# Performance work log

Measured on AMD Instinct MI355X. Metric: run time of the kernel, lower is better.

Reference implementation:

```python
import jax, jax.numpy as jnp
import numpy as np

N = 50000   # input points
E = 800000  # edges
M = 25000   # sampled points (ratio 0.5)
K = 15      # num_neighbors
H = 128     # hidden_dim
BN_EPS = 1e-5


def setup_inputs() -> dict:
    key = jax.random.key(0)
    ks = jax.random.split(key, 16)
    w = lambda k, s: jax.random.normal(k, s, dtype=jnp.float32) * 0.02
    z = lambda s: jnp.zeros(s, jnp.float32)
    o = lambda s: jnp.ones(s, jnp.float32)
    return {
        'points': jax.random.normal(ks[0], (N, 3), jnp.float32),
        'edge_index': jax.random.randint(ks[1], (2, E), 0, N),
        'sampled_idx': jnp.sort(jax.random.randint(ks[2], (M,), 0, N)),
        'neighbors': jax.random.randint(ks[3], (M, K), 0, M),
        'W1': w(ks[4], (3, H)), 'b1': z(H), 'g1': o(H), 'beta1': z(H),
        'W2': w(ks[5], (H, H)), 'b2': z(H), 'g2': o(H), 'beta2': z(H),
        'Wc': w(ks[6], (H, H)), 'bc': z(H),
        'Wn': w(ks[7], (H, H)), 'bn_b': z(H),
        'Wq': w(ks[8], (H, H // 2)), 'bq': z(H // 2),
        'Wk': w(ks[9], (H, H // 2)), 'bk': z(H // 2),
        'Wcat': w(ks[10], (H + 3, H + 3)), 'bcat': z(H + 3),
        'Wout': w(ks[11], (H + 3, 3)), 'bout': z(3),
    }


def _bn(x, g, b):
    # BatchNorm1d in training mode: batch mean, biased batch var
    m = x.mean(axis=0)
    v = x.var(axis=0)
    return g * (x - m) * jax.lax.rsqrt(v + BN_EPS) + b


def reference(points, edge_index, sampled_idx, neighbors,
              W1, b1, g1, beta1, W2, b2, g2, beta2,
              Wc, bc, Wn, bn_b, Wq, bq, Wk, bk, Wcat, bcat, Wout, bout):
    n = points.shape[0]
    # PointMLP x2: Linear -> BN -> ReLU
    x = jax.nn.relu(_bn(points @ W1 + b1, g1, beta1))
    x = jax.nn.relu(_bn(x @ W2 + b2, g2, beta2))
    # CustomGNN: relu(W_c x + mean_{j in N(i)} W_n x_j)
    src, dst = edge_index[0], edge_index[1]
    msg = (x @ Wn + bn_b)[src]                                   # [E, H]
    agg = jax.ops.segment_sum(msg, dst, num_segments=n)          # [N, H]
    cnt = jax.ops.segment_sum(jnp.ones(src.shape, jnp.float32), dst, num_segments=n)
    agg = agg / jnp.maximum(cnt, 1.0)[:, None]
    x = jax.nn.relu(x @ Wc + bc + agg)
    # sampling (indices precomputed, like fps output)
    sp = points[sampled_idx]                                     # [M, 3]
    sx = x[sampled_idx]                                          # [M, H]
    # AttentionLayer, fully vectorized over sampled points
    q = sx @ Wq + bq                                             # [M, H/2]
    nb_x = sx[neighbors]                                         # [M, K, H]
    k = nb_x @ Wk + bk                                           # [M, K, H/2]
    scale = jnp.sqrt(jnp.float32(q.shape[-1])) + 1e-6
    scores = jnp.einsum('md,mkd->mk', q, k) / scale              # [M, K]
    mask = (neighbors != 0).astype(jnp.float32)                  # quirk preserved
    attn = jax.nn.softmax(scores * mask, axis=1)                 # [M, K]
    rel = sp[neighbors] - sp[:, None, :]                         # [M, K, 3]
    cat = jnp.concatenate([nb_x, rel], axis=-1)                  # [M, K, H+3]
    proc = cat @ Wcat + bcat                                     # [M, K, H+3]
    aggf = jnp.einsum('mk,mkd->md', attn, proc)                  # [M, H+3]
    disp = aggf @ Wout + bout                                    # [M, 3]
    refined = sp + disp
    return refined, sx
```

## Files before the change

### kernel.cpp

```cpp
#include <hip/hip_runtime.h>
#include <climits>

#define NPTS 50000
#define NE   800000
#define MS   25000
#define KN   15
#define HD   128

__device__ __forceinline__ float wave_sum(float v) {
#pragma unroll
    for (int o = 32; o > 0; o >>= 1) v += __shfl_xor(v, o, 64);
    return v;
}

__launch_bounds__(256)
__global__ void prep_kernel(const float* __restrict__ Wq, const float* __restrict__ bq,
                            const float* __restrict__ Wk, const float* __restrict__ bk,
                            const float* __restrict__ Wcat, const float* __restrict__ bcat,
                            const float* __restrict__ Wout, const float* __restrict__ bout,
                            const float* __restrict__ Wc, const float* __restrict__ Wn,
                            float* __restrict__ Wqk, float* __restrict__ biasQK,
                            float* __restrict__ WcWn,
                            float* __restrict__ Wco128, float* __restrict__ w3, float* __restrict__ bco,
                            int* __restrict__ inv, int* __restrict__ cnt, int* __restrict__ cursor) {
    int b = blockIdx.x, tid = threadIdx.x;
    if (b < 64) {
        int i = b * 256 + tid;
        int k = i >> 7, c = i & 127;
        Wqk[i] = (c < 64) ? Wq[k * 64 + c] : Wk[k * 64 + (c - 64)];
    } else if (b < 192) {
        int i = (b - 64) * 256 + tid;
        int k = i >> 7, c = i & 127;
        WcWn[i] = (k < 128) ? Wc[k * 128 + c] : Wn[(k - 128) * 128 + c];
    } else if (b == 192) {
        if (tid < 128) biasQK[tid] = (tid < 64) ? bq[tid] : bk[tid - 64];
    } else if (b < 293) {
        int wid = tid >> 6, lane = tid & 63;
        int out = (b - 193) * 4 + wid;
        if (out < 396) {
            int r = out / 3, j = out - r * 3;
            const float* src = (r < 131) ? &Wcat[r * 131] : bcat;
            float s = 0.f;
            s = fmaf(src[lane], Wout[lane * 3 + j], s);
            s = fmaf(src[lane + 64], Wout[(lane + 64) * 3 + j], s);
            if (lane < 3) s = fmaf(src[lane + 128], Wout[(lane + 128) * 3 + j], s);
            s = wave_sum(s);
            if (lane == 0) {
                if (r < 128) Wco128[r * 3 + j] = s;
                else if (r < 131) w3[(r - 128) * 3 + j] = s;
                else bco[j] = s + bout[j];
            }
        }
    } else {
        int i = (b - 293) * 256 + tid;
        if (i < NPTS) inv[i] = INT_MAX;
        if (i < MS) { cnt[i] = 0; cursor[i] = 0; }
    }
}

__launch_bounds__(256)
__global__ void lin1_kernel(const float* __restrict__ pts, const float* __restrict__ W1,
                            const float* __restrict__ b1, float* __restrict__ y1,
                            float* __restrict__ psum, float* __restrict__ psq,
                            const int* __restrict__ smp, int* __restrict__ inv) {
    if (blockIdx.x >= 1000) {
        int m = (blockIdx.x - 1000) * 256 + threadIdx.x;
        if (m < MS) atomicMin(&inv[smp[m]], m);
        return;
    }
    int c = threadIdx.x & 127;
    int half = threadIdx.x >> 7;
    int part = blockIdx.x * 2 + half;
    float w0 = W1[c], w1 = W1[128 + c], w2 = W1[256 + c], bb = b1[c];
    float s = 0.f, s2 = 0.f;
    int r0 = part * 25, r1 = r0 + 25; if (r1 > NPTS) r1 = NPTS;
    for (int r = r0; r < r1; ++r) {
        float p0 = pts[r * 3], p1 = pts[r * 3 + 1], p2 = pts[r * 3 + 2];
        float y = fmaf(p0, w0, fmaf(p1, w1, fmaf(p2, w2, bb)));
        y1[r * HD + c] = y;
        s += y; s2 = fmaf(y, y, s2);
    }
    psum[part * 128 + c] = s;
    psq[part * 128 + c] = s2;
}

__launch_bounds__(256)
__global__ void bn_fin_par(const float* __restrict__ psum, const float* __restrict__ psq, int nb,
                           const float* __restrict__ g, const float* __restrict__ beta,
                           float* __restrict__ tp) {
    int c = blockIdx.x;
    int t = threadIdx.x;
    float S = 0.f, S2 = 0.f;
    for (int b = t; b < nb; b += 256) {
        S += psum[b * 128 + c];
        S2 += psq[b * 128 + c];
    }
    S = wave_sum(S); S2 = wave_sum(S2);
    __shared__ float sA[4], sB[4];
    int wid = t >> 6, lane = t & 63;
    if (lane == 0) { sA[wid] = S; sB[wid] = S2; }
    __syncthreads();
    if (t == 0) {
        float Sa = sA[0] + sA[1] + sA[2] + sA[3];
        float Sb = sB[0] + sB[1] + sB[2] + sB[3];
        const float invN = 1.f / (float)NPTS;
        float mean = Sa * invN;
        float var = Sb * invN - mean * mean;
        float a = g[c] * rsqrtf(var + 1e-5f);
        tp[c] = a;
        tp[128 + c] = beta[c] - mean * a;
    }
}

template <int R, bool TRANS, bool STATS, bool COUNT>
__launch_bounds__(256)
__global__ void gemm_bn(const float* __restrict__ A, int nrows, int gemmBlocks,
                        const float* __restrict__ W, const float* __restrict__ bias,
                        const float* __restrict__ tp,
                        float* __restrict__ Out,
                        float* __restrict__ psum, float* __restrict__ psq,
                        const int* __restrict__ ei, const int* __restrict__ inv,
                        int* __restrict__ cnt) {
    if (COUNT && (int)blockIdx.x >= gemmBlocks) {
        int e = ((int)blockIdx.x - gemmBlocks) * 256 + threadIdx.x;
        if (e < NE) {
            int mr = inv[ei[NE + e]];
            if (mr < MS) atomicAdd(&cnt[mr], 1);
        }
        return;
    }
    const int ROWS = 8 * R;
    __shared__ float As[8 * R][68];
    __shared__ float Ws[64][128];
    int tid = threadIdx.x;
    int r0 = blockIdx.x * ROWS;
    int tc = tid & 31, tr = tid >> 5;
    int trR = tr * R, c0 = tc << 2;
    float acc[R][4] = {};

    for (int k0 = 0; k0 < 128; k0 += 64) {
        if (k0) __syncthreads();
        for (int i = tid; i < ROWS * 16; i += 256) {
            int r = i >> 4, c4 = (i & 15) << 2;
            int gr = r0 + r;
            float4 v = make_float4(0.f, 0.f, 0.f, 0.f);
            if (gr < nrows) {
                v = *reinterpret_cast<const float4*>(&A[gr * HD + k0 + c4]);
                if (TRANS) {
                    int gc = k0 + c4;
                    v.x = fmaxf(fmaf(tp[gc],     v.x, tp[128 + gc]),     0.f);
                    v.y = fmaxf(fmaf(tp[gc + 1], v.y, tp[128 + gc + 1]), 0.f);
                    v.z = fmaxf(fmaf(tp[gc + 2], v.z, tp[128 + gc + 2]), 0.f);
                    v.w = fmaxf(fmaf(tp[gc + 3], v.w, tp[128 + gc + 3]), 0.f);
                }
            }
            *reinterpret_cast<float4*>(&As[r][c4]) = v;
        }
        for (int i = tid; i < 64 * 32; i += 256) {
            int k = i >> 5, c4 = (i & 31) << 2;
            *reinterpret_cast<float4*>(&Ws[k][c4]) =
                *reinterpret_cast<const float4*>(&W[(k0 + k) * 128 + c4]);
        }
        __syncthreads();
#pragma unroll 2
        for (int k = 0; k < 64; k += 4) {
            float4 a[R];
#pragma unroll
            for (int i = 0; i < R; ++i)
                a[i] = *reinterpret_cast<const float4*>(&As[trR + i][k]);
#pragma unroll
            for (int kk = 0; kk < 4; ++kk) {
                const float4 wv = *reinterpret_cast<const float4*>(&Ws[k + kk][c0]);
#pragma unroll
                for (int i = 0; i < R; ++i) {
                    float av = kk == 0 ? a[i].x : kk == 1 ? a[i].y : kk == 2 ? a[i].z : a[i].w;
                    acc[i][0] = fmaf(av, wv.x, acc[i][0]);
                    acc[i][1] = fmaf(av, wv.y, acc[i][1]);
                    acc[i][2] = fmaf(av, wv.z, acc[i][2]);
                    acc[i][3] = fmaf(av, wv.w, acc[i][3]);
                }
            }
        }
    }

    const float4 bv = *reinterpret_cast<const float4*>(&bias[c0]);
    float cs[4] = {}, cq[4] = {};
#pragma unroll
    for (int i = 0; i < R; ++i) {
        int gr = r0 + trR + i;
        float o0 = acc[i][0] + bv.x, o1 = acc[i][1] + bv.y;
        float o2 = acc[i][2] + bv.z, o3 = acc[i][3] + bv.w;
        if (gr < nrows) {
            *reinterpret_cast<float4*>(&Out[gr * HD + c0]) = make_float4(o0, o1, o2, o3);
            if (STATS) {
                cs[0] += o0; cs[1] += o1; cs[2] += o2; cs[3] += o3;
                cq[0] = fmaf(o0, o0, cq[0]); cq[1] = fmaf(o1, o1, cq[1]);
                cq[2] = fmaf(o2, o2, cq[2]); cq[3] = fmaf(o3, o3, cq[3]);
            }
        }
    }
    if (STATS) {
        float* red = &As[0][0];
        __syncthreads();
        *reinterpret_cast<float4*>(&red[tr * 128 + c0]) = make_float4(cs[0], cs[1], cs[2], cs[3]);
        __syncthreads();
        if (tid < 128) {
            float s = 0.f;
#pragma unroll
            for (int t = 0; t < 8; ++t) s += red[t * 128 + tid];
            psum[blockIdx.x * 128 + tid] = s;
        }
        __syncthreads();
        *reinterpret_cast<float4*>(&red[tr * 128 + c0]) = make_float4(cq[0], cq[1], cq[2], cq[3]);
        __syncthreads();
        if (tid < 128) {
            float s = 0.f;
#pragma unroll
            for (int t = 0; t < 8; ++t) s += red[t * 128 + tid];
            psq[blockIdx.x * 128 + tid] = s;
        }
    }
}

__launch_bounds__(1024)
__global__ void scan_kernel(const int* __restrict__ cnt, int* __restrict__ offs) {
    const int C = 25;
    __shared__ int buf[1024];
    int tid = threadIdx.x;
    int loc[C];
    int run = 0;
    int base = tid * C;
#pragma unroll
    for (int i = 0; i < C; ++i) {
        int idx = base + i;
        int v = (idx < MS) ? cnt[idx] : 0;
        loc[i] = run; run += v;
    }
    buf[tid] = run;
    __syncthreads();
    for (int off = 1; off < 1024; off <<= 1) {
        int t = (tid >= off) ? buf[tid - off] : 0;
        __syncthreads();
        buf[tid] += t;
        __syncthreads();
    }
    int excl = buf[tid] - run;
#pragma unroll
    for (int i = 0; i < C; ++i) {
        int idx = base + i;
        if (idx < MS) offs[idx] = excl + loc[i];
    }
    if (tid == 1023) offs[MS] = buf[tid];
}

__launch_bounds__(256)
__global__ void scatter_kernel(const int* __restrict__ ei, const int* __restrict__ inv,
                               const int* __restrict__ offs, int* __restrict__ cursor,
                               int* __restrict__ elist) {
    int e = blockIdx.x * 256 + threadIdx.x;
    if (e < NE) {
        int mr = inv[ei[NE + e]];
        if (mr < MS) {
            int pos = atomicAdd(&cursor[mr], 1);
            elist[offs[mr] + pos] = ei[e];
        }
    }
}

__launch_bounds__(256)
__global__ void agg_kernel(const int* __restrict__ smp, const int* __restrict__ inv,
                           const int* __restrict__ offs, const int* __restrict__ elist,
                           const float* __restrict__ y2, const float* __restrict__ tp2,
                           float* __restrict__ aggX, float* __restrict__ hasE) {
    int tid = threadIdx.x, wid = tid >> 6, lane = tid & 63;
    int m = blockIdx.x * 4 + wid;
    if (m >= MS) return;
    int d = smp[m];
    if (inv[d] != m) return;
    int half = lane >> 5, c0 = (lane & 31) << 2;
    const float4 ta = *reinterpret_cast<const float4*>(&tp2[c0]);
    const float4 tb = *reinterpret_cast<const float4*>(&tp2[128 + c0]);
    int e0 = offs[m], e1 = offs[m + 1];
    float4 s0 = {0,0,0,0}, s1 = {0,0,0,0}, s2 = {0,0,0,0}, s3 = {0,0,0,0};
    int e = e0;
    for (; e + 7 < e1; e += 8) {
        float4 v[4];
#pragma unroll
        for (int u = 0; u < 4; ++u)
            v[u] = *reinterpret_cast<const float4*>(&y2[elist[e + 2 * u + half] * HD + c0]);
        s0.x += fmaxf(fmaf(ta.x, v[0].x, tb.x), 0.f); s0.y += fmaxf(fmaf(ta.y, v[0].y, tb.y), 0.f);
        s0.z += fmaxf(fmaf(ta.z, v[0].z, tb.z), 0.f); s0.w += fmaxf(fmaf(ta.w, v[0].w, tb.w), 0.f);
        s1.x += fmaxf(fmaf(ta.x, v[1].x, tb.x), 0.f); s1.y += fmaxf(fmaf(ta.y, v[1].y, tb.y), 0.f);
        s1.z += fmaxf(fmaf(ta.z, v[1].z, tb.z), 0.f); s1.w += fmaxf(fmaf(ta.w, v[1].w, tb.w), 0.f);
        s2.x += fmaxf(fmaf(ta.x, v[2].x, tb.x), 0.f); s2.y += fmaxf(fmaf(ta.y, v[2].y, tb.y), 0.f);
        s2.z += fmaxf(fmaf(ta.z, v[2].z, tb.z), 0.f); s2.w += fmaxf(fmaf(ta.w, v[2].w, tb.w), 0.f);
        s3.x += fmaxf(fmaf(ta.x, v[3].x, tb.x), 0.f); s3.y += fmaxf(fmaf(ta.y, v[3].y, tb.y), 0.f);
        s3.z += fmaxf(fmaf(ta.z, v[3].z, tb.z), 0.f); s3.w += fmaxf(fmaf(ta.w, v[3].w, tb.w), 0.f);
    }
    for (; e + 1 < e1; e += 2) {
        const float4 v = *reinterpret_cast<const float4*>(&y2[elist[e + half] * HD + c0]);
        s0.x += fmaxf(fmaf(ta.x, v.x, tb.x), 0.f); s0.y += fmaxf(fmaf(ta.y, v.y, tb.y), 0.f);
        s0.z += fmaxf(fmaf(ta.z, v.z, tb.z), 0.f); s0.w += fmaxf(fmaf(ta.w, v.w, tb.w), 0.f);
    }
    if (e < e1 && half == 0) {
        const float4 v = *reinterpret_cast<const float4*>(&y2[elist[e] * HD + c0]);
        s1.x += fmaxf(fmaf(ta.x, v.x, tb.x), 0.f); s1.y += fmaxf(fmaf(ta.y, v.y, tb.y), 0.f);
        s1.z += fmaxf(fmaf(ta.z, v.z, tb.z), 0.f); s1.w += fmaxf(fmaf(ta.w, v.w, tb.w), 0.f);
    }
    float tx = (s0.x + s1.x) + (s2.x + s3.x);
    float ty = (s0.y + s1.y) + (s2.y + s3.y);
    float tz = (s0.z + s1.z) + (s2.z + s3.z);
    float tw = (s0.w + s1.w) + (s2.w + s3.w);
    tx += __shfl_xor(tx, 32, 64); ty += __shfl_xor(ty, 32, 64);
    tz += __shfl_xor(tz, 32, 64); tw += __shfl_xor(tw, 32, 64);
    float rs = 1.f / fmaxf((float)(e1 - e0), 1.f);
    if (half == 0)
        *reinterpret_cast<float4*>(&aggX[m * HD + c0]) = make_float4(tx * rs, ty * rs, tz * rs, tw * rs);
    if (lane == 0) hasE[m] = (e1 > e0) ? 1.f : 0.f;
}

__launch_bounds__(256)
__global__ void gemm_sx_fused(const float* __restrict__ y2, const float* __restrict__ aggX,
                              const float* __restrict__ hasE,
                              const int* __restrict__ smp, const int* __restrict__ inv,
                              const float* __restrict__ WcWn,
                              const float* __restrict__ bc, const float* __restrict__ bn_b,
                              const float* __restrict__ tp2,
                              const float* __restrict__ Wqk, const float* __restrict__ biasQK,
                              const float* __restrict__ Wco128, const float* __restrict__ pts,
                              float* __restrict__ sx, float* __restrict__ qkb,
                              float* __restrict__ p3, float* __restrict__ sp) {
    const int R = 3;
    __shared__ float As[24][68];
    __shared__ float Ws[64][128];
    __shared__ float sxs[24][132];
    int tid = threadIdx.x;
    int r0 = blockIdx.x * 24;
    int tc = tid & 31, tr = tid >> 5;
    int trR = tr * R, c0 = tc << 2;
    float acc[R][4] = {};

    for (int kk = 0; kk < 4; ++kk) {
        if (kk) __syncthreads();
        for (int i = tid; i < 24 * 16; i += 256) {
            int r = i >> 4, c4 = (i & 15) << 2;
            int gr = r0 + r;
            float4 v = make_float4(0.f, 0.f, 0.f, 0.f);
            if (gr < MS) {
                int d = smp[gr];
                if (kk < 2) {
                    int gc = (kk << 6) + c4;
                    v = *reinterpret_cast<const float4*>(&y2[d * HD + gc]);
                    v.x = fmaxf(fmaf(tp2[gc],     v.x, tp2[128 + gc]),     0.f);
                    v.y = fmaxf(fmaf(tp2[gc + 1], v.y, tp2[128 + gc + 1]), 0.f);
                    v.z = fmaxf(fmaf(tp2[gc + 2], v.z, tp2[128 + gc + 2]), 0.f);
                    v.w = fmaxf(fmaf(tp2[gc + 3], v.w, tp2[128 + gc + 3]), 0.f);
                } else {
                    v = *reinterpret_cast<const float4*>(&aggX[inv[d] * HD + ((kk - 2) << 6) + c4]);
                }
            }
            *reinterpret_cast<float4*>(&As[r][c4]) = v;
        }
        for (int i = tid; i < 64 * 32; i += 256) {
            int k = i >> 5, c4 = (i & 31) << 2;
            *reinterpret_cast<float4*>(&Ws[k][c4]) =
                *reinterpret_cast<const float4*>(&WcWn[((kk << 6) + k) * 128 + c4]);
        }
        __syncthreads();
#pragma unroll 2
        for (int k = 0; k < 64; k += 4) {
            float4 a[R];
#pragma unroll
            for (int i = 0; i < R; ++i)
                a[i] = *reinterpret_cast<const float4*>(&As[trR + i][k]);
#pragma unroll
            for (int kq = 0; kq < 4; ++kq) {
                const float4 wv = *reinterpret_cast<const float4*>(&Ws[k + kq][c0]);
#pragma unroll
                for (int i = 0; i < R; ++i) {
                    float av = kq == 0 ? a[i].x : kq == 1 ? a[i].y : kq == 2 ? a[i].z : a[i].w;
                    acc[i][0] = fmaf(av, wv.x, acc[i][0]);
                    acc[i][1] = fmaf(av, wv.y, acc[i][1]);
                    acc[i][2] = fmaf(av, wv.z, acc[i][2]);
                    acc[i][3] = fmaf(av, wv.w, acc[i][3]);
                }
            }
        }
    }

    {
        const float4 bcv = *reinterpret_cast<const float4*>(&bc[c0]);
        const float4 bnv = *reinterpret_cast<const float4*>(&bn_b[c0]);
#pragma unroll
        for (int i = 0; i < R; ++i) {
            int gr = r0 + trR + i;
            float4 ov = make_float4(0.f, 0.f, 0.f, 0.f);
            if (gr < MS) {
                float f = hasE[inv[smp[gr]]];
                ov.x = fmaxf(acc[i][0] + bcv.x + f * bnv.x, 0.f);
                ov.y = fmaxf(acc[i][1] + bcv.y + f * bnv.y, 0.f);
                ov.z = fmaxf(acc[i][2] + bcv.z + f * bnv.z, 0.f);
                ov.w = fmaxf(acc[i][3] + bcv.w + f * bnv.w, 0.f);
                *reinterpret_cast<float4*>(&sx[gr * HD + c0]) = ov;
            }
            *reinterpret_cast<float4*>(&sxs[trR + i][c0]) = ov;
        }
    }
    __syncthreads();

    float qacc[R][4] = {};
    for (int kk = 0; kk < 2; ++kk) {
        if (kk) __syncthreads();
        for (int i = tid; i < 64 * 32; i += 256) {
            int k = i >> 5, c4 = (i & 31) << 2;
            *reinterpret_cast<float4*>(&Ws[k][c4]) =
                *reinterpret_cast<const float4*>(&Wqk[((kk << 6) + k) * 128 + c4]);
        }
        __syncthreads();
        int kb = kk << 6;
#pragma unroll 2
        for (int k = 0; k < 64; k += 4) {
            float4 a[R];
#pragma unroll
            for (int i = 0; i < R; ++i)
                a[i] = *reinterpret_cast<const float4*>(&sxs[trR + i][kb + k]);
#pragma unroll
            for (int kq = 0; kq < 4; ++kq) {
                const float4 wv = *reinterpret_cast<const float4*>(&Ws[k + kq][c0]);
#pragma unroll
                for (int i = 0; i < R; ++i) {
                    float av = kq == 0 ? a[i].x : kq == 1 ? a[i].y : kq == 2 ? a[i].z : a[i].w;
                    qacc[i][0] = fmaf(av, wv.x, qacc[i][0]);
                    qacc[i][1] = fmaf(av, wv.y, qacc[i][1]);
                    qacc[i][2] = fmaf(av, wv.z, qacc[i][2]);
                    qacc[i][3] = fmaf(av, wv.w, qacc[i][3]);
                }
            }
        }
    }
    {
        const float4 bqv = *reinterpret_cast<const float4*>(&biasQK[c0]);
#pragma unroll
        for (int i = 0; i < R; ++i) {
            int gr = r0 + trR + i;
            if (gr < MS) {
                *reinterpret_cast<float4*>(&qkb[gr * HD + c0]) = make_float4(
                    qacc[i][0] + bqv.x, qacc[i][1] + bqv.y,
                    qacc[i][2] + bqv.z, qacc[i][3] + bqv.w);
            }
        }
    }

    {
        int wid = tid >> 6, lane = tid & 63;
        int cc = lane << 1;
        float wa0 = Wco128[cc * 3],     wa1 = Wco128[cc * 3 + 1],     wa2 = Wco128[cc * 3 + 2];
        float wb0 = Wco128[(cc+1) * 3], wb1 = Wco128[(cc+1) * 3 + 1], wb2 = Wco128[(cc+1) * 3 + 2];
#pragma unroll
        for (int rr = wid * 6; rr < wid * 6 + 6; ++rr) {
            int m = r0 + rr;
            if (m >= MS) break;
            float vx = sxs[rr][cc], vy = sxs[rr][cc + 1];
            float q0 = fmaf(vx, wa0, vy * wb0);
            float q1 = fmaf(vx, wa1, vy * wb1);
            float q2 = fmaf(vx, wa2, vy * wb2);
            q0 = wave_sum(q0); q1 = wave_sum(q1); q2 = wave_sum(q2);
            if (lane == 0) { p3[m * 3] = q0; p3[m * 3 + 1] = q1; p3[m * 3 + 2] = q2; }
            if (lane < 3) sp[m * 3 + lane] = pts[smp[m] * 3 + lane];
        }
    }
}

__launch_bounds__(256)
__global__ void attn_kernel(const float* __restrict__ qk, const int* __restrict__ nbr,
                            const float* __restrict__ p3, const float* __restrict__ sp,
                            const float* __restrict__ w3, const float* __restrict__ bco,
                            float* __restrict__ refined) {
    int wid = threadIdx.x >> 6, lane = threadIdx.x & 63;
    int m = blockIdx.x * 4 + wid;
    if (m >= MS) return;
    float ql = qk[m * HD + lane];
    int nbv[KN];
    float s[KN];
#pragma unroll
    for (int j = 0; j < KN; ++j) nbv[j] = nbr[m * KN + j];
#pragma unroll
    for (int j = 0; j < KN; ++j) {
        float t = ql * qk[nbv[j] * HD + 64 + lane];
        t = wave_sum(t);
        s[j] = (nbv[j] != 0) ? t * (1.f / 8.000001f) : 0.f;
    }
    float mx = s[0];
#pragma unroll
    for (int j = 1; j < KN; ++j) mx = fmaxf(mx, s[j]);
    float den = 0.f;
#pragma unroll
    for (int j = 0; j < KN; ++j) { s[j] = __expf(s[j] - mx); den += s[j]; }
    float invd = 1.f / den;
    float sp0 = sp[m * 3], sp1 = sp[m * 3 + 1], sp2 = sp[m * 3 + 2];
    float a0 = 0.f, a1 = 0.f, a2 = 0.f;
#pragma unroll
    for (int j = 0; j < KN; ++j) {
        int nb = nbv[j];
        float wgt = s[j] * invd;
        float r0 = sp[nb * 3] - sp0, r1 = sp[nb * 3 + 1] - sp1, r2 = sp[nb * 3 + 2] - sp2;
        float g0 = p3[nb * 3]     + r0 * w3[0] + r1 * w3[3] + r2 * w3[6];
        float g1 = p3[nb * 3 + 1] + r0 * w3[1] + r1 * w3[4] + r2 * w3[7];
        float g2 = p3[nb * 3 + 2] + r0 * w3[2] + r1 * w3[5] + r2 * w3[8];
        a0 = fmaf(wgt, g0, a0); a1 = fmaf(wgt, g1, a1); a2 = fmaf(wgt, g2, a2);
    }
    if (lane == 0) {
        refined[m * 3]     = sp0 + a0 + bco[0];
        refined[m * 3 + 1] = sp1 + a1 + bco[1];
        refined[m * 3 + 2] = sp2 + a2 + bco[2];
    }
}

extern "C" void kernel_launch(void* const* d_in, const int* in_sizes, int n_in,
                              void* d_out, int out_size, void* d_ws, size_t ws_size,
                              hipStream_t stream) {
    const float* pts   = (const float*)d_in[0];
    const int*   ei    = (const int*)d_in[1];
    const int*   smp   = (const int*)d_in[2];
    const int*   nbr   = (const int*)d_in[3];
    const float* W1    = (const float*)d_in[4];
    const float* b1    = (const float*)d_in[5];
    const float* g1    = (const float*)d_in[6];
    const float* beta1 = (const float*)d_in[7];
    const float* W2    = (const float*)d_in[8];
    const float* b2    = (const float*)d_in[9];
    const float* g2    = (const float*)d_in[10];
    const float* beta2 = (const float*)d_in[11];
    const float* Wc    = (const float*)d_in[12];
    const float* bc    = (const float*)d_in[13];
    const float* Wn    = (const float*)d_in[14];
    const float* bn_b  = (const float*)d_in[15];
    const float* Wq    = (const float*)d_in[16];
    const float* bq    = (const float*)d_in[17];
    const float* Wk    = (const float*)d_in[18];
    const float* bk    = (const float*)d_in[19];
    const float* Wcat  = (const float*)d_in[20];
    const float* bcat  = (const float*)d_in[21];
    const float* Wout  = (const float*)d_in[22];
    const float* bout  = (const float*)d_in[23];
    (void)in_sizes; (void)n_in; (void)out_size; (void)ws_size;

    float* w = (float*)d_ws;
    size_t o = 0;
    float* y1     = w + o; o += 6400000;
    float* y2     = w + o; o += 6400000;
    float* aggX   = w + o; o += 3200000;
    float* qkb    = w + o; o += 3200000;
    float* psum   = w + o; o += 262144;
    float* psq    = w + o; o += 262144;
    float* tp1    = w + o; o += 256;
    float* tp2    = w + o; o += 256;
    float* Wqk    = w + o; o += 16384;
    float* biasQK = w + o; o += 128;
    float* WcWn   = w + o; o += 32768;
    float* Wco128 = w + o; o += 384;
    float* w3     = w + o; o += 16;
    float* bco    = w + o; o += 16;
    float* p3     = w + o; o += 75008;
    float* sp     = w + o; o += 75008;
    float* hasE   = w + o; o += 25008;
    int* ip    = (int*)(w + o);
    int* inv   = ip;            ip += NPTS;
    int* cnt   = ip;            ip += MS;
    int* cursor= ip;            ip += MS;
    int* offs  = ip;            ip += MS + 4;
    int* elist = ip;

    float* refined = (float*)d_out;
    float* sx      = (float*)d_out + 75000;

    prep_kernel<<<489, 256, 0, stream>>>(Wq, bq, Wk, bk, Wcat, bcat, Wout, bout, Wc, Wn,
                                         Wqk, biasQK, WcWn, Wco128, w3, bco,
                                         inv, cnt, cursor);
    lin1_kernel<<<1098, 256, 0, stream>>>(pts, W1, b1, y1, psum, psq, smp, inv);
    bn_fin_par<<<128, 256, 0, stream>>>(psum, psq, 2000, g1, beta1, tp1);
    gemm_bn<6, true, true, true><<<1042 + 3125, 256, 0, stream>>>(
        y1, NPTS, 1042, W2, b2, tp1, y2, psum, psq, ei, inv, cnt);
    bn_fin_par<<<128, 256, 0, stream>>>(psum, psq, 1042, g2, beta2, tp2);
    scan_kernel<<<1, 1024, 0, stream>>>(cnt, offs);
    scatter_kernel<<<3125, 256, 0, stream>>>(ei, inv, offs, cursor, elist);
    agg_kernel<<<6250, 256, 0, stream>>>(smp, inv, offs, elist, y2, tp2, aggX, hasE);
    gemm_sx_fused<<<1042, 256, 0, stream>>>(y2, aggX, hasE, smp, inv, WcWn, bc, bn_b, tp2,
                                            Wqk, biasQK, Wco128, pts, sx, qkb, p3, sp);
    attn_kernel<<<6250, 256, 0, stream>>>(qkb, nbr, p3, sp, w3, bco, refined);
}
```

Measured before the change: 321.6 us.

## Recompute first linear layer inside second GEMM and enlarge GEMM row tiles

The first point linear layer no longer writes its 50000x128 output; it only produces BN statistics, and the second GEMM recomputes it from the 3-D points on the fly before applying BN and ReLU. This removes a large global write and read of y1 in exchange for a little extra arithmetic per tile load. The y2 GEMM tile grows from 48 to 64 rows and the sx fused GEMM from 24 to 32 rows, reusing the sxs shared buffer as the A tile to save shared memory. The larger tiles raise register pressure and reduce block count.

```diff
diff --git a/kernel.cpp b/kernel.cpp
--- a/kernel.cpp
+++ b/kernel.cpp
@@ -59,10 +59,10 @@
 }
 
 __launch_bounds__(256)
-__global__ void lin1_kernel(const float* __restrict__ pts, const float* __restrict__ W1,
-                            const float* __restrict__ b1, float* __restrict__ y1,
-                            float* __restrict__ psum, float* __restrict__ psq,
-                            const int* __restrict__ smp, int* __restrict__ inv) {
+__global__ void lin1_stats(const float* __restrict__ pts, const float* __restrict__ W1,
+                           const float* __restrict__ b1,
+                           float* __restrict__ psum, float* __restrict__ psq,
+                           const int* __restrict__ smp, int* __restrict__ inv) {
     if (blockIdx.x >= 1000) {
         int m = (blockIdx.x - 1000) * 256 + threadIdx.x;
         if (m < MS) atomicMin(&inv[smp[m]], m);
@@ -77,7 +77,6 @@
     for (int r = r0; r < r1; ++r) {
         float p0 = pts[r * 3], p1 = pts[r * 3 + 1], p2 = pts[r * 3 + 2];
         float y = fmaf(p0, w0, fmaf(p1, w1, fmaf(p2, w2, bb)));
-        y1[r * HD + c] = y;
         s += y; s2 = fmaf(y, y, s2);
     }
     psum[part * 128 + c] = s;
@@ -112,16 +111,16 @@
     }
 }
 
-template <int R, bool TRANS, bool STATS, bool COUNT>
-__launch_bounds__(256)
-__global__ void gemm_bn(const float* __restrict__ A, int nrows, int gemmBlocks,
-                        const float* __restrict__ W, const float* __restrict__ bias,
-                        const float* __restrict__ tp,
-                        float* __restrict__ Out,
+__launch_bounds__(256)
+__global__ void gemm_y2(const float* __restrict__ pts, const float* __restrict__ W1,
+                        const float* __restrict__ b1, const float* __restrict__ tp1,
+                        const float* __restrict__ W2, const float* __restrict__ b2,
+                        int gemmBlocks,
+                        float* __restrict__ y2,
                         float* __restrict__ psum, float* __restrict__ psq,
                         const int* __restrict__ ei, const int* __restrict__ inv,
                         int* __restrict__ cnt) {
-    if (COUNT && (int)blockIdx.x >= gemmBlocks) {
+    if ((int)blockIdx.x >= gemmBlocks) {
         int e = ((int)blockIdx.x - gemmBlocks) * 256 + threadIdx.x;
         if (e < NE) {
             int mr = inv[ei[NE + e]];
@@ -129,50 +128,57 @@
         }
         return;
     }
-    const int ROWS = 8 * R;
-    __shared__ float As[8 * R][68];
+    __shared__ float As[64][68];
     __shared__ float Ws[64][128];
     int tid = threadIdx.x;
-    int r0 = blockIdx.x * ROWS;
+    int r0 = blockIdx.x * 64;
     int tc = tid & 31, tr = tid >> 5;
-    int trR = tr * R, c0 = tc << 2;
-    float acc[R][4] = {};
+    int trR = tr * 8, c0 = tc << 2;
+    float acc[8][4] = {};
 
     for (int k0 = 0; k0 < 128; k0 += 64) {
         if (k0) __syncthreads();
-        for (int i = tid; i < ROWS * 16; i += 256) {
+        for (int i = tid; i < 64 * 16; i += 256) {
             int r = i >> 4, c4 = (i & 15) << 2;
             int gr = r0 + r;
             float4 v = make_float4(0.f, 0.f, 0.f, 0.f);
-            if (gr < nrows) {
-                v = *reinterpret_cast<const float4*>(&A[gr * HD + k0 + c4]);
-                if (TRANS) {
-                    int gc = k0 + c4;
-                    v.x = fmaxf(fmaf(tp[gc],     v.x, tp[128 + gc]),     0.f);
-                    v.y = fmaxf(fmaf(tp[gc + 1], v.y, tp[128 + gc + 1]), 0.f);
-                    v.z = fmaxf(fmaf(tp[gc + 2], v.z, tp[128 + gc + 2]), 0.f);
-                    v.w = fmaxf(fmaf(tp[gc + 3], v.w, tp[128 + gc + 3]), 0.f);
-                }
+            if (gr < NPTS) {
+                int gc = k0 + c4;
+                float p0 = pts[gr * 3], p1 = pts[gr * 3 + 1], p2 = pts[gr * 3 + 2];
+                const float4 wa = *reinterpret_cast<const float4*>(&W1[gc]);
+                const float4 wb = *reinterpret_cast<const float4*>(&W1[128 + gc]);
+                const float4 wc = *reinterpret_cast<const float4*>(&W1[256 + gc]);
+                const float4 bb = *reinterpret_cast<const float4*>(&b1[gc]);
+                const float4 ta = *reinterpret_cast<const float4*>(&tp1[gc]);
+                const float4 tb = *reinterpret_cast<const float4*>(&tp1[128 + gc]);
+                float y0 = fmaf(p0, wa.x, fmaf(p1, wb.x, fmaf(p2, wc.x, bb.x)));
+                float y1v = fmaf(p0, wa.y, fmaf(p1, wb.y, fmaf(p2, wc.y, bb.y)));
+                float y2v = fmaf(p0, wa.z, fmaf(p1, wb.z, fmaf(p2, wc.z, bb.z)));
+                float y3 = fmaf(p0, wa.w, fmaf(p1, wb.w, fmaf(p2, wc.w, bb.w)));
+                v.x = fmaxf(fmaf(ta.x, y0,  tb.x), 0.f);
+                v.y = fmaxf(fmaf(ta.y, y1v, tb.y), 0.f);
+                v.z = fmaxf(fmaf(ta.z, y2v, tb.z), 0.f);
+                v.w = fmaxf(fmaf(ta.w, y3,  tb.w), 0.f);
             }
             *reinterpret_cast<float4*>(&As[r][c4]) = v;
         }
         for (int i = tid; i < 64 * 32; i += 256) {
             int k = i >> 5, c4 = (i & 31) << 2;
             *reinterpret_cast<float4*>(&Ws[k][c4]) =
-                *reinterpret_cast<const float4*>(&W[(k0 + k) * 128 + c4]);
+                *reinterpret_cast<const float4*>(&W2[(k0 + k) * 128 + c4]);
         }
         __syncthreads();
 #pragma unroll 2
         for (int k = 0; k < 64; k += 4) {
-            float4 a[R];
-#pragma unroll
-            for (int i = 0; i < R; ++i)
+            float4 a[8];
+#pragma unroll
+            for (int i = 0; i < 8; ++i)
                 a[i] = *reinterpret_cast<const float4*>(&As[trR + i][k]);
 #pragma unroll
             for (int kk = 0; kk < 4; ++kk) {
                 const float4 wv = *reinterpret_cast<const float4*>(&Ws[k + kk][c0]);
 #pragma unroll
-                for (int i = 0; i < R; ++i) {
+                for (int i = 0; i < 8; ++i) {
                     float av = kk == 0 ? a[i].x : kk == 1 ? a[i].y : kk == 2 ? a[i].z : a[i].w;
                     acc[i][0] = fmaf(av, wv.x, acc[i][0]);
                     acc[i][1] = fmaf(av, wv.y, acc[i][1]);
@@ -183,42 +189,38 @@
         }
     }
 
-    const float4 bv = *reinterpret_cast<const float4*>(&bias[c0]);
+    const float4 bv = *reinterpret_cast<const float4*>(&b2[c0]);
     float cs[4] = {}, cq[4] = {};
 #pragma unroll
-    for (int i = 0; i < R; ++i) {
+    for (int i = 0; i < 8; ++i) {
         int gr = r0 + trR + i;
         float o0 = acc[i][0] + bv.x, o1 = acc[i][1] + bv.y;
         float o2 = acc[i][2] + bv.z, o3 = acc[i][3] + bv.w;
-        if (gr < nrows) {
-            *reinterpret_cast<float4*>(&Out[gr * HD + c0]) = make_float4(o0, o1, o2, o3);
-            if (STATS) {
-                cs[0] += o0; cs[1] += o1; cs[2] += o2; cs[3] += o3;
-                cq[0] = fmaf(o0, o0, cq[0]); cq[1] = fmaf(o1, o1, cq[1]);
-                cq[2] = fmaf(o2, o2, cq[2]); cq[3] = fmaf(o3, o3, cq[3]);
-            }
-        }
-    }
-    if (STATS) {
-        float* red = &As[0][0];
-        __syncthreads();
-        *reinterpret_cast<float4*>(&red[tr * 128 + c0]) = make_float4(cs[0], cs[1], cs[2], cs[3]);
-        __syncthreads();
-        if (tid < 128) {
-            float s = 0.f;
-#pragma unroll
-            for (int t = 0; t < 8; ++t) s += red[t * 128 + tid];
-            psum[blockIdx.x * 128 + tid] = s;
-        }
-        __syncthreads();
-        *reinterpret_cast<float4*>(&red[tr * 128 + c0]) = make_float4(cq[0], cq[1], cq[2], cq[3]);
-        __syncthreads();
-        if (tid < 128) {
-            float s = 0.f;
-#pragma unroll
-            for (int t = 0; t < 8; ++t) s += red[t * 128 + tid];
-            psq[blockIdx.x * 128 + tid] = s;
-        }
+        if (gr < NPTS) {
+            *reinterpret_cast<float4*>(&y2[gr * HD + c0]) = make_float4(o0, o1, o2, o3);
+            cs[0] += o0; cs[1] += o1; cs[2] += o2; cs[3] += o3;
+            cq[0] = fmaf(o0, o0, cq[0]); cq[1] = fmaf(o1, o1, cq[1]);
+            cq[2] = fmaf(o2, o2, cq[2]); cq[3] = fmaf(o3, o3, cq[3]);
+        }
+    }
+    float* red = &As[0][0];
+    __syncthreads();
+    *reinterpret_cast<float4*>(&red[tr * 128 + c0]) = make_float4(cs[0], cs[1], cs[2], cs[3]);
+    __syncthreads();
+    if (tid < 128) {
+        float s = 0.f;
+#pragma unroll
+        for (int t = 0; t < 8; ++t) s += red[t * 128 + tid];
+        psum[blockIdx.x * 128 + tid] = s;
+    }
+    __syncthreads();
+    *reinterpret_cast<float4*>(&red[tr * 128 + c0]) = make_float4(cq[0], cq[1], cq[2], cq[3]);
+    __syncthreads();
+    if (tid < 128) {
+        float s = 0.f;
+#pragma unroll
+        for (int t = 0; t < 8; ++t) s += red[t * 128 + tid];
+        psq[blockIdx.x * 128 + tid] = s;
     }
 }
 
@@ -330,19 +332,17 @@
                               const float* __restrict__ Wco128, const float* __restrict__ pts,
                               float* __restrict__ sx, float* __restrict__ qkb,
                               float* __restrict__ p3, float* __restrict__ sp) {
-    const int R = 3;
-    __shared__ float As[24][68];
     __shared__ float Ws[64][128];
-    __shared__ float sxs[24][132];
+    __shared__ float sxs[32][132];
     int tid = threadIdx.x;
-    int r0 = blockIdx.x * 24;
+    int r0 = blockIdx.x * 32;
     int tc = tid & 31, tr = tid >> 5;
-    int trR = tr * R, c0 = tc << 2;
-    float acc[R][4] = {};
+    int trR = tr * 4, c0 = tc << 2;
+    float acc[4][4] = {};
 
     for (int kk = 0; kk < 4; ++kk) {
         if (kk) __syncthreads();
-        for (int i = tid; i < 24 * 16; i += 256) {
+        for (int i = tid; i < 32 * 16; i += 256) {
             int r = i >> 4, c4 = (i & 15) << 2;
             int gr = r0 + r;
             float4 v = make_float4(0.f, 0.f, 0.f, 0.f);
@@ -359,7 +359,7 @@
                     v = *reinterpret_cast<const float4*>(&aggX[inv[d] * HD + ((kk - 2) << 6) + c4]);
                 }
             }
-            *reinterpret_cast<float4*>(&As[r][c4]) = v;
+            *reinterpret_cast<float4*>(&sxs[r][c4]) = v;
         }
         for (int i = tid; i < 64 * 32; i += 256) {
             int k = i >> 5, c4 = (i & 31) << 2;
@@ -369,15 +369,15 @@
         __syncthreads();
 #pragma unroll 2
         for (int k = 0; k < 64; k += 4) {
-            float4 a[R];
-#pragma unroll
-            for (int i = 0; i < R; ++i)
-                a[i] = *reinterpret_cast<const float4*>(&As[trR + i][k]);
+            float4 a[4];
+#pragma unroll
+            for (int i = 0; i < 4; ++i)
+                a[i] = *reinterpret_cast<const float4*>(&sxs[trR + i][k]);
 #pragma unroll
             for (int kq = 0; kq < 4; ++kq) {
                 const float4 wv = *reinterpret_cast<const float4*>(&Ws[k + kq][c0]);
 #pragma unroll
-                for (int i = 0; i < R; ++i) {
+                for (int i = 0; i < 4; ++i) {
                     float av = kq == 0 ? a[i].x : kq == 1 ? a[i].y : kq == 2 ? a[i].z : a[i].w;
                     acc[i][0] = fmaf(av, wv.x, acc[i][0]);
                     acc[i][1] = fmaf(av, wv.y, acc[i][1]);
@@ -388,11 +388,12 @@
         }
     }
 
+    __syncthreads();
     {
         const float4 bcv = *reinterpret_cast<const float4*>(&bc[c0]);
         const float4 bnv = *reinterpret_cast<const float4*>(&bn_b[c0]);
 #pragma unroll
-        for (int i = 0; i < R; ++i) {
+        for (int i = 0; i < 4; ++i) {
             int gr = r0 + trR + i;
             float4 ov = make_float4(0.f, 0.f, 0.f, 0.f);
             if (gr < MS) {
@@ -408,7 +409,7 @@
     }
     __syncthreads();
 
-    float qacc[R][4] = {};
+    float qacc[4][4] = {};
     for (int kk = 0; kk < 2; ++kk) {
         if (kk) __syncthreads();
         for (int i = tid; i < 64 * 32; i += 256) {
@@ -420,15 +421,15 @@
         int kb = kk << 6;
 #pragma unroll 2
         for (int k = 0; k < 64; k += 4) {
-            float4 a[R];
-#pragma unroll
-            for (int i = 0; i < R; ++i)
+            float4 a[4];
+#pragma unroll
+            for (int i = 0; i < 4; ++i)
                 a[i] = *reinterpret_cast<const float4*>(&sxs[trR + i][kb + k]);
 #pragma unroll
             for (int kq = 0; kq < 4; ++kq) {
                 const float4 wv = *reinterpret_cast<const float4*>(&Ws[k + kq][c0]);
 #pragma unroll
-                for (int i = 0; i < R; ++i) {
+                for (int i = 0; i < 4; ++i) {
                     float av = kq == 0 ? a[i].x : kq == 1 ? a[i].y : kq == 2 ? a[i].z : a[i].w;
                     qacc[i][0] = fmaf(av, wv.x, qacc[i][0]);
                     qacc[i][1] = fmaf(av, wv.y, qacc[i][1]);
@@ -441,7 +442,7 @@
     {
         const float4 bqv = *reinterpret_cast<const float4*>(&biasQK[c0]);
 #pragma unroll
-        for (int i = 0; i < R; ++i) {
+        for (int i = 0; i < 4; ++i) {
             int gr = r0 + trR + i;
             if (gr < MS) {
                 *reinterpret_cast<float4*>(&qkb[gr * HD + c0]) = make_float4(
@@ -457,7 +458,7 @@
         float wa0 = Wco128[cc * 3],     wa1 = Wco128[cc * 3 + 1],     wa2 = Wco128[cc * 3 + 2];
         float wb0 = Wco128[(cc+1) * 3], wb1 = Wco128[(cc+1) * 3 + 1], wb2 = Wco128[(cc+1) * 3 + 2];
 #pragma unroll
-        for (int rr = wid * 6; rr < wid * 6 + 6; ++rr) {
+        for (int rr = wid * 8; rr < wid * 8 + 8; ++rr) {
             int m = r0 + rr;
             if (m >= MS) break;
             float vx = sxs[rr][cc], vy = sxs[rr][cc + 1];
@@ -570,6 +571,7 @@
     int* cursor= ip;            ip += MS;
     int* offs  = ip;            ip += MS + 4;
     int* elist = ip;
+    (void)y1;
 
     float* refined = (float*)d_out;
     float* sx      = (float*)d_out + 75000;
@@ -577,15 +579,15 @@
     prep_kernel<<<489, 256, 0, stream>>>(Wq, bq, Wk, bk, Wcat, bcat, Wout, bout, Wc, Wn,
                                          Wqk, biasQK, WcWn, Wco128, w3, bco,
                                          inv, cnt, cursor);
-    lin1_kernel<<<1098, 256, 0, stream>>>(pts, W1, b1, y1, psum, psq, smp, inv);
+    lin1_stats<<<1098, 256, 0, stream>>>(pts, W1, b1, psum, psq, smp, inv);
     bn_fin_par<<<128, 256, 0, stream>>>(psum, psq, 2000, g1, beta1, tp1);
-    gemm_bn<6, true, true, true><<<1042 + 3125, 256, 0, stream>>>(
-        y1, NPTS, 1042, W2, b2, tp1, y2, psum, psq, ei, inv, cnt);
-    bn_fin_par<<<128, 256, 0, stream>>>(psum, psq, 1042, g2, beta2, tp2);
+    gemm_y2<<<782 + 3125, 256, 0, stream>>>(pts, W1, b1, tp1, W2, b2, 782,
+                                            y2, psum, psq, ei, inv, cnt);
+    bn_fin_par<<<128, 256, 0, stream>>>(psum, psq, 782, g2, beta2, tp2);
     scan_kernel<<<1, 1024, 0, stream>>>(cnt, offs);
     scatter_kernel<<<3125, 256, 0, stream>>>(ei, inv, offs, cursor, elist);
     agg_kernel<<<6250, 256, 0, stream>>>(smp, inv, offs, elist, y2, tp2, aggX, hasE);
-    gemm_sx_fused<<<1042, 256, 0, stream>>>(y2, aggX, hasE, smp, inv, WcWn, bc, bn_b, tp2,
-                                            Wqk, biasQK, Wco128, pts, sx, qkb, p3, sp);
+    gemm_sx_fused<<<782, 256, 0, stream>>>(y2, aggX, hasE, smp, inv, WcWn, bc, bn_b, tp2,
+                                           Wqk, biasQK, Wco128, pts, sx, qkb, p3, sp);
     attn_kernel<<<6250, 256, 0, stream>>>(qkb, nbr, p3, sp, w3, bco, refined);
 }
```

Measured after the change: 327.6 us. About the same (+1.9%).
